# Performance work log

Measured on AMD Instinct MI355X. Metric: run time of the kernel, lower is better.

Reference implementation:

```python
import jax, jax.numpy as jnp
import numpy as np
import math

D_MODEL = 2048
D_STATE = 16
EXPAND = 2
D_INNER = D_MODEL * EXPAND          # 4096
DT_RANK = math.ceil(D_MODEL / 16)   # 128
BATCH, SEQ_LEN = 2, 512


def setup_inputs() -> dict:
    key = jax.random.key(0)
    ks = jax.random.split(key, 6)
    x = jax.random.normal(ks[0], (BATCH, SEQ_LEN, D_INNER), dtype=jnp.float32)
    # A_log such that A = -exp(A_log) is a stable negative-real decay
    A_log = jnp.log(jax.random.uniform(ks[1], (D_INNER, D_STATE), minval=0.5, maxval=16.0, dtype=jnp.float32))
    D = jnp.ones((D_INNER,), dtype=jnp.float32)
    x_proj_w = 0.02 * jax.random.normal(ks[2], (DT_RANK + 2 * D_STATE, D_INNER), dtype=jnp.float32)
    dt_init_std = DT_RANK ** -0.5
    dt_proj_w = jax.random.uniform(ks[3], (D_INNER, DT_RANK), minval=-dt_init_std, maxval=dt_init_std, dtype=jnp.float32)
    # inverse-softplus init of dt bias, dt ~ loguniform[1e-3, 0.1]
    dt = jnp.exp(jax.random.uniform(ks[4], (D_INNER,), dtype=jnp.float32) * (math.log(0.1) - math.log(0.001)) + math.log(0.001))
    dt = jnp.clip(dt, 1e-4, None)
    dt_proj_b = dt + jnp.log(-jnp.expm1(-dt))
    return {"x": x, "A_log": A_log, "D": D, "x_proj_w": x_proj_w,
            "dt_proj_w": dt_proj_w, "dt_proj_b": dt_proj_b}


def reference(x, A_log, D, x_proj_w, dt_proj_w, dt_proj_b):
    # x: (b, l, d)
    A = -jnp.exp(A_log)                                  # (d, n)
    xp = jnp.einsum('bld,rd->blr', x, x_proj_w)          # (b, l, dt_rank + 2n)
    dt_in = xp[..., :DT_RANK]
    B = xp[..., DT_RANK:DT_RANK + D_STATE]               # (b, l, n)
    C = xp[..., DT_RANK + D_STATE:]                      # (b, l, n)
    dt = jax.nn.softplus(jnp.einsum('blr,dr->bld', dt_in, dt_proj_w) + dt_proj_b)  # (b, l, d)
    dA = jnp.exp(dt[..., None] * A)                      # (b, l, d, n)
    dBx = dt[..., None] * B[:, :, None, :] * x[..., None]  # (b, l, d, n)

    def step(h, inp):
        dA_t, dBx_t, C_t = inp                           # (b,d,n), (b,d,n), (b,n)
        h = dA_t * h + dBx_t
        y = jnp.einsum('bdn,bn->bd', h, C_t)
        return h, y

    h0 = jnp.zeros((x.shape[0], D_INNER, D_STATE), dtype=x.dtype)
    _, ys = jax.lax.scan(step, h0,
                         (jnp.moveaxis(dA, 1, 0), jnp.moveaxis(dBx, 1, 0), jnp.moveaxis(C, 1, 0)))
    y = jnp.moveaxis(ys, 0, 1) + D * x                   # (b, l, d)
    return y
```

## Files before the change

### kernel.cpp

```cpp
#include <hip/hip_runtime.h>
#include <math.h>

#define BATCH   2
#define SEQLEN  512
#define DI      4096
#define DS      16
#define RDT     128
#define RTOT    160
#define BL      1024

#define KSPLIT  32
#define KSL     (DI / KSPLIT)

typedef __bf16 bf16;
typedef bf16  bf16x8 __attribute__((ext_vector_type(8)));
typedef bf16  bf16x4 __attribute__((ext_vector_type(4)));
typedef float f32x4  __attribute__((ext_vector_type(4)));

__global__ __launch_bounds__(256) void cast_both(const float* __restrict__ W,
                                                 const float* __restrict__ dtw,
                                                 bf16* __restrict__ Wb,
                                                 bf16* __restrict__ dtwb) {
  const int i = blockIdx.x * 256 + threadIdx.x;
  const float4* src;
  bf16* dst;
  int j;
  if (i < RTOT * DI / 4) { src = (const float4*)W;   dst = Wb;   j = i; }
  else                   { src = (const float4*)dtw; dst = dtwb; j = i - RTOT * DI / 4; }
  float4 v = src[j];
  bf16x4 o;
  o[0] = (bf16)v.x; o[1] = (bf16)v.y; o[2] = (bf16)v.z; o[3] = (bf16)v.w;
  *(bf16x4*)(dst + 4 * (size_t)j) = o;
}

__global__ __launch_bounds__(256) void gemm_xp_mfma(const float* __restrict__ x,
                                                    const bf16* __restrict__ Wb,
                                                    float* __restrict__ part) {
  const int tid = threadIdx.x;
  const int w = tid >> 6;
  const int lane = tid & 63;
  const int m = lane & 15;
  const int q = lane >> 4;
  const int row0 = blockIdx.x * 64 + 16 * w;
  const int k0 = blockIdx.y * KSL;

  f32x4 acc[10] = {};

  const float* ap = x + (size_t)(row0 + m) * DI + k0 + 8 * q;
  const bf16*  bp = Wb + (size_t)m * DI + k0 + 8 * q;

#pragma unroll
  for (int kk = 0; kk < KSL; kk += 32) {
    float4 a0 = *(const float4*)(ap + kk);
    float4 a1 = *(const float4*)(ap + kk + 4);
    bf16x8 af;
    af[0] = (bf16)a0.x; af[1] = (bf16)a0.y; af[2] = (bf16)a0.z; af[3] = (bf16)a0.w;
    af[4] = (bf16)a1.x; af[5] = (bf16)a1.y; af[6] = (bf16)a1.z; af[7] = (bf16)a1.w;
#pragma unroll
    for (int nt = 0; nt < 10; ++nt) {
      bf16x8 bfv = *(const bf16x8*)(bp + (size_t)nt * 16 * DI + kk);
      acc[nt] = __builtin_amdgcn_mfma_f32_16x16x32_bf16(af, bfv, acc[nt], 0, 0, 0);
    }
  }

  float* p = part + (size_t)blockIdx.y * (BL * RTOT);
#pragma unroll
  for (int nt = 0; nt < 10; ++nt)
#pragma unroll
    for (int r = 0; r < 4; ++r)
      p[(size_t)(row0 + 4 * q + r) * RTOT + nt * 16 + m] = acc[nt][r];
}

__global__ __launch_bounds__(256) void reduce_xp(const float* __restrict__ part,
                                                 float* __restrict__ BCf,
                                                 bf16* __restrict__ dtinb) {
  const int o = (blockIdx.x * 256 + threadIdx.x) * 4;
  float4 s = make_float4(0.f, 0.f, 0.f, 0.f);
#pragma unroll
  for (int k = 0; k < KSPLIT; ++k) {
    float4 v = *(const float4*)&part[(size_t)k * (BL * RTOT) + o];
    s.x += v.x; s.y += v.y; s.z += v.z; s.w += v.w;
  }
  const int row = o / RTOT;
  const int col = o - row * RTOT;
  if (col < RDT) {
    bf16x4 ob;
    ob[0] = (bf16)s.x; ob[1] = (bf16)s.y; ob[2] = (bf16)s.z; ob[3] = (bf16)s.w;
    *(bf16x4*)(dtinb + (size_t)row * RDT + col) = ob;
  } else {
    *(float4*)&BCf[(size_t)row * 32 + (col - RDT)] = s;
  }
}

__device__ __forceinline__ float row16_reduce_add(float p) {
  p += __int_as_float(__builtin_amdgcn_update_dpp(
      0, __float_as_int(p), 0x111, 0xf, 0xf, true));
  p += __int_as_float(__builtin_amdgcn_update_dpp(
      0, __float_as_int(p), 0x112, 0xf, 0xf, true));
  p += __int_as_float(__builtin_amdgcn_update_dpp(
      0, __float_as_int(p), 0x114, 0xf, 0xf, true));
  p += __int_as_float(__builtin_amdgcn_update_dpp(
      0, __float_as_int(p), 0x118, 0xf, 0xf, true));
  return p;
}

#define TC  64
#define TCP 68
#define NCH (SEQLEN / TC)

__global__ __launch_bounds__(256) void scan_fused(const float* __restrict__ x,
                                                  const float* __restrict__ A_log,
                                                  const float* __restrict__ Dvec,
                                                  const float* __restrict__ BCf,
                                                  const bf16* __restrict__ dtin,
                                                  const bf16* __restrict__ dtwb,
                                                  const float* __restrict__ dtb,
                                                  float* __restrict__ out) {
  __shared__ __align__(16) float dtS[16][TCP];
  __shared__ __align__(16) float xS[16][TCP];
  __shared__ __align__(16) float BS[16][TCP];
  __shared__ __align__(16) float CS[16][TCP];
  __shared__ __align__(16) float yS[TC][16];

  const int bid = blockIdx.x;
  const int b = bid >> 8;
  const int d0 = (bid & 255) * 16;
  const int tid = threadIdx.x;
  const int n = tid & 15;
  const int dc = tid >> 4;
  const int d = d0 + dc;
  const int w = tid >> 6;
  const int m = tid & 15;
  const int q = (tid >> 4) & 3;

  const float A = -expf(A_log[d * DS + n]);
  const float Dd = Dvec[d];
  const float bias = dtb[d0 + m];

  bf16x8 bfragW[4];
#pragma unroll
  for (int k = 0; k < 4; ++k)
    bfragW[k] = *(const bf16x8*)(dtwb + (size_t)(d0 + m) * RDT + 32 * k + 8 * q);

  const int lt = tid >> 2;
  const int lf = (tid & 3) * 4;
  const int rowbase = b * SEQLEN;

  bf16x8 afrag[4];
  float4 rx, rB, rC;
  {
    const int arow = rowbase + 16 * w + m;
#pragma unroll
    for (int k = 0; k < 4; ++k)
      afrag[k] = *(const bf16x8*)(dtin + (size_t)arow * RDT + 32 * k + 8 * q);
    const int row = rowbase + lt;
    rx = *(const float4*)&x[(size_t)row * DI + d0 + lf];
    rB = *(const float4*)&BCf[row * 32 + lf];
    rC = *(const float4*)&BCf[row * 32 + 16 + lf];
  }

  float h = 0.f;

  for (int c = 0; c < NCH; ++c) {
    if (c > 0) __syncthreads();

    {
      f32x4 acc = {};
#pragma unroll
      for (int k = 0; k < 4; ++k)
        acc = __builtin_amdgcn_mfma_f32_16x16x32_bf16(afrag[k], bfragW[k], acc, 0, 0, 0);
#pragma unroll
      for (int r = 0; r < 4; ++r) {
        const float z = acc[r] + bias;
        dtS[m][16 * w + 4 * q + r] = (z > 20.f) ? z : __logf(1.f + __expf(z));
      }
    }
    {
      const float rxa[4] = {rx.x, rx.y, rx.z, rx.w};
      const float rBa[4] = {rB.x, rB.y, rB.z, rB.w};
      const float rCa[4] = {rC.x, rC.y, rC.z, rC.w};
#pragma unroll
      for (int j = 0; j < 4; ++j) {
        xS[lf + j][lt] = rxa[j];
        BS[lf + j][lt] = rBa[j];
        CS[lf + j][lt] = rCa[j];
      }
    }
    if (c > 0) {
      const int prow = rowbase + (c - 1) * TC + lt;
      float4 yv = *(const float4*)&yS[lt][lf];
      *(float4*)&out[(size_t)prow * DI + d0 + lf] = yv;
    }

    __syncthreads();

    if (c < NCH - 1) {
      const int arow = rowbase + (c + 1) * TC + 16 * w + m;
#pragma unroll
      for (int k = 0; k < 4; ++k)
        afrag[k] = *(const bf16x8*)(dtin + (size_t)arow * RDT + 32 * k + 8 * q);
      const int row = rowbase + (c + 1) * TC + lt;
      rx = *(const float4*)&x[(size_t)row * DI + d0 + lf];
      rB = *(const float4*)&BCf[row * 32 + lf];
      rC = *(const float4*)&BCf[row * 32 + 16 + lf];
    }

    for (int g = 0; g < 8; ++g) {
      const int t0 = 8 * g;
      const float4 dv0 = *(const float4*)&dtS[dc][t0];
      const float4 dv1 = *(const float4*)&dtS[dc][t0 + 4];
      const float4 xv0 = *(const float4*)&xS[dc][t0];
      const float4 xv1 = *(const float4*)&xS[dc][t0 + 4];
      const float4 Bv0 = *(const float4*)&BS[n][t0];
      const float4 Bv1 = *(const float4*)&BS[n][t0 + 4];
      const float4 Cv0 = *(const float4*)&CS[n][t0];
      const float4 Cv1 = *(const float4*)&CS[n][t0 + 4];
      const float dt[8] = {dv0.x, dv0.y, dv0.z, dv0.w, dv1.x, dv1.y, dv1.z, dv1.w};
      const float xv[8] = {xv0.x, xv0.y, xv0.z, xv0.w, xv1.x, xv1.y, xv1.z, xv1.w};
      const float Bv[8] = {Bv0.x, Bv0.y, Bv0.z, Bv0.w, Bv1.x, Bv1.y, Bv1.z, Bv1.w};
      const float Cv[8] = {Cv0.x, Cv0.y, Cv0.z, Cv0.w, Cv1.x, Cv1.y, Cv1.z, Cv1.w};

      float e[8], u[8], p[8];
#pragma unroll
      for (int j = 0; j < 8; ++j) {
        e[j] = __expf(dt[j] * A);
        u[j] = dt[j] * xv[j] * Bv[j];
      }
#pragma unroll
      for (int j = 0; j < 8; ++j) {
        h = fmaf(e[j], h, u[j]);
        p[j] = h * Cv[j];
      }
#pragma unroll
      for (int j = 0; j < 8; ++j)
        p[j] = row16_reduce_add(p[j]);
      if (n == 15) {
#pragma unroll
        for (int j = 0; j < 8; ++j)
          yS[t0 + j][dc] = fmaf(Dd, xv[j], p[j]);
      }
    }
  }

  __syncthreads();
  {
    const int prow = rowbase + (NCH - 1) * TC + lt;
    float4 yv = *(const float4*)&yS[lt][lf];
    *(float4*)&out[(size_t)prow * DI + d0 + lf] = yv;
  }
}

extern "C" void kernel_launch(void* const* d_in, const int* in_sizes, int n_in,
                              void* d_out, int out_size, void* d_ws, size_t ws_size,
                              hipStream_t stream) {
  const float* x     = (const float*)d_in[0];
  const float* A_log = (const float*)d_in[1];
  const float* Dv    = (const float*)d_in[2];
  const float* W     = (const float*)d_in[3];
  const float* dtw   = (const float*)d_in[4];
  const float* dtb   = (const float*)d_in[5];
  float* out = (float*)d_out;

  char* ws = (char*)d_ws;
  float* part  = (float*)ws;
  bf16*  Wb    = (bf16*)(ws + 20971520);
  bf16*  dtwb  = (bf16*)(ws + 22282240);
  float* BCf   = (float*)(ws + 23330816);
  bf16*  dtinb = (bf16*)(ws + 23461888);

  cast_both<<<dim3(1152), 256, 0, stream>>>(W, dtw, Wb, dtwb);
  gemm_xp_mfma<<<dim3(16, KSPLIT), 256, 0, stream>>>(x, Wb, part);
  reduce_xp<<<dim3(160), 256, 0, stream>>>(part, BCf, dtinb);
  scan_fused<<<dim3(512), 256, 0, stream>>>(x, A_log, Dv, BCf, dtinb, dtwb, dtb, out);
}
```

Before: 137.6 us.

## Replace split-K partials and reduce kernel with in-block reduction plus atomics

Drops the weight cast kernel and the separate split-K reduction. The GEMM now converts fp32 weights to bf16 in registers, reduces its four waves' partial sums through shared memory, and atomically adds the result into a zeroed fp32 xp buffer. This removes the 20MB partial-sum write and read. The scan reads fp32 xp directly, converts it to bf16 per chunk, and folds log2e into the weights and A so it can use exp2/log2, and it fully unrolls the inner group loop. The atomics make summation order nondeterministic, and the scan now reloads wider fp32 fragments.

Measured after the change: 147.3 us. 1.07x slower.

```diff
diff --git a/kernel.cpp b/kernel.cpp
--- a/kernel.cpp
+++ b/kernel.cpp
@@ -9,86 +9,81 @@
 #define RTOT    160
 #define BL      1024
 
-#define KSPLIT  32
-#define KSL     (DI / KSPLIT)
+#define LOG2E 1.44269504088896340736f
+#define LN2   0.69314718055994530942f
 
 typedef __bf16 bf16;
 typedef bf16  bf16x8 __attribute__((ext_vector_type(8)));
-typedef bf16  bf16x4 __attribute__((ext_vector_type(4)));
 typedef float f32x4  __attribute__((ext_vector_type(4)));
 
-__global__ __launch_bounds__(256) void cast_both(const float* __restrict__ W,
-                                                 const float* __restrict__ dtw,
-                                                 bf16* __restrict__ Wb,
-                                                 bf16* __restrict__ dtwb) {
+__device__ __forceinline__ bf16x8 cvt8(const float4 a, const float4 b) {
+  bf16x8 r;
+  r[0] = (bf16)a.x; r[1] = (bf16)a.y; r[2] = (bf16)a.z; r[3] = (bf16)a.w;
+  r[4] = (bf16)b.x; r[5] = (bf16)b.y; r[6] = (bf16)b.z; r[7] = (bf16)b.w;
+  return r;
+}
+
+__device__ __forceinline__ bf16x8 cvt8s(const float4 a, const float4 b, const float s) {
+  bf16x8 r;
+  r[0] = (bf16)(s * a.x); r[1] = (bf16)(s * a.y); r[2] = (bf16)(s * a.z); r[3] = (bf16)(s * a.w);
+  r[4] = (bf16)(s * b.x); r[5] = (bf16)(s * b.y); r[6] = (bf16)(s * b.z); r[7] = (bf16)(s * b.w);
+  return r;
+}
+
+__global__ __launch_bounds__(256) void zero_xp(float* __restrict__ xp) {
   const int i = blockIdx.x * 256 + threadIdx.x;
-  const float4* src;
-  bf16* dst;
-  int j;
-  if (i < RTOT * DI / 4) { src = (const float4*)W;   dst = Wb;   j = i; }
-  else                   { src = (const float4*)dtw; dst = dtwb; j = i - RTOT * DI / 4; }
-  float4 v = src[j];
-  bf16x4 o;
-  o[0] = (bf16)v.x; o[1] = (bf16)v.y; o[2] = (bf16)v.z; o[3] = (bf16)v.w;
-  *(bf16x4*)(dst + 4 * (size_t)j) = o;
-}
-
-__global__ __launch_bounds__(256) void gemm_xp_mfma(const float* __restrict__ x,
-                                                    const bf16* __restrict__ Wb,
-                                                    float* __restrict__ part) {
+  *(float4*)&xp[4 * (size_t)i] = make_float4(0.f, 0.f, 0.f, 0.f);
+}
+
+#define MT    16
+#define KS    8
+#define LPAD  168
+
+__global__ __launch_bounds__(256, 2) void gemm_xp(const float* __restrict__ x,
+                                                  const float* __restrict__ W,
+                                                  float* __restrict__ xp) {
+  __shared__ float Lred[4][MT * LPAD];
   const int tid = threadIdx.x;
   const int w = tid >> 6;
   const int lane = tid & 63;
   const int m = lane & 15;
   const int q = lane >> 4;
-  const int row0 = blockIdx.x * 64 + 16 * w;
-  const int k0 = blockIdx.y * KSL;
+  const int row0 = blockIdx.x * MT;
+  const int k0 = blockIdx.y * (DI / KS) + w * 128;
 
   f32x4 acc[10] = {};
-
   const float* ap = x + (size_t)(row0 + m) * DI + k0 + 8 * q;
-  const bf16*  bp = Wb + (size_t)m * DI + k0 + 8 * q;
-
-#pragma unroll
-  for (int kk = 0; kk < KSL; kk += 32) {
+  const float* wp = W + (size_t)m * DI + k0 + 8 * q;
+
+#pragma unroll
+  for (int kk = 0; kk < 128; kk += 32) {
     float4 a0 = *(const float4*)(ap + kk);
     float4 a1 = *(const float4*)(ap + kk + 4);
-    bf16x8 af;
-    af[0] = (bf16)a0.x; af[1] = (bf16)a0.y; af[2] = (bf16)a0.z; af[3] = (bf16)a0.w;
-    af[4] = (bf16)a1.x; af[5] = (bf16)a1.y; af[6] = (bf16)a1.z; af[7] = (bf16)a1.w;
+    bf16x8 af = cvt8(a0, a1);
 #pragma unroll
     for (int nt = 0; nt < 10; ++nt) {
-      bf16x8 bfv = *(const bf16x8*)(bp + (size_t)nt * 16 * DI + kk);
-      acc[nt] = __builtin_amdgcn_mfma_f32_16x16x32_bf16(af, bfv, acc[nt], 0, 0, 0);
-    }
-  }
-
-  float* p = part + (size_t)blockIdx.y * (BL * RTOT);
+      const float* wq = wp + (size_t)nt * 16 * DI + kk;
+      float4 b0 = *(const float4*)(wq);
+      float4 b1 = *(const float4*)(wq + 4);
+      acc[nt] = __builtin_amdgcn_mfma_f32_16x16x32_bf16(af, cvt8(b0, b1), acc[nt], 0, 0, 0);
+    }
+  }
+
 #pragma unroll
   for (int nt = 0; nt < 10; ++nt)
 #pragma unroll
     for (int r = 0; r < 4; ++r)
-      p[(size_t)(row0 + 4 * q + r) * RTOT + nt * 16 + m] = acc[nt][r];
-}
-
-__global__ __launch_bounds__(256) void reduce_xp(const float* __restrict__ part,
-                                                 float* __restrict__ BCf,
-                                                 bf16* __restrict__ dtinb) {
-  const int o = (blockIdx.x * 256 + threadIdx.x) * 4;
-  float4 s = make_float4(0.f, 0.f, 0.f, 0.f);
-#pragma unroll
-  for (int k = 0; k < KSPLIT; ++k) {
-    float4 v = *(const float4*)&part[(size_t)k * (BL * RTOT) + o];
-    s.x += v.x; s.y += v.y; s.z += v.z; s.w += v.w;
-  }
-  const int row = o / RTOT;
-  const int col = o - row * RTOT;
-  if (col < RDT) {
-    bf16x4 ob;
-    ob[0] = (bf16)s.x; ob[1] = (bf16)s.y; ob[2] = (bf16)s.z; ob[3] = (bf16)s.w;
-    *(bf16x4*)(dtinb + (size_t)row * RDT + col) = ob;
-  } else {
-    *(float4*)&BCf[(size_t)row * 32 + (col - RDT)] = s;
+      Lred[w][(4 * q + r) * LPAD + nt * 16 + m] = acc[nt][r];
+  __syncthreads();
+
+#pragma unroll
+  for (int i = 0; i < 10; ++i) {
+    const int o = i * 256 + tid;
+    const int row = o / 160;
+    const int col = o - row * 160;
+    const int a = row * LPAD + col;
+    const float s = Lred[0][a] + Lred[1][a] + Lred[2][a] + Lred[3][a];
+    unsafeAtomicAdd(&xp[(size_t)(row0 + row) * RTOT + col], s);
   }
 }
 
@@ -108,14 +103,13 @@
 #define TCP 68
 #define NCH (SEQLEN / TC)
 
-__global__ __launch_bounds__(256) void scan_fused(const float* __restrict__ x,
-                                                  const float* __restrict__ A_log,
-                                                  const float* __restrict__ Dvec,
-                                                  const float* __restrict__ BCf,
-                                                  const bf16* __restrict__ dtin,
-                                                  const bf16* __restrict__ dtwb,
-                                                  const float* __restrict__ dtb,
-                                                  float* __restrict__ out) {
+__global__ __launch_bounds__(256, 2) void scan_fused(const float* __restrict__ x,
+                                                     const float* __restrict__ A_log,
+                                                     const float* __restrict__ Dvec,
+                                                     const float* __restrict__ xp,
+                                                     const float* __restrict__ dtw,
+                                                     const float* __restrict__ dtb,
+                                                     float* __restrict__ out) {
   __shared__ __align__(16) float dtS[16][TCP];
   __shared__ __align__(16) float xS[16][TCP];
   __shared__ __align__(16) float BS[16][TCP];
@@ -133,30 +127,37 @@
   const int m = tid & 15;
   const int q = (tid >> 4) & 3;
 
-  const float A = -expf(A_log[d * DS + n]);
+  const float A2 = -LOG2E * __expf(A_log[d * DS + n]);
   const float Dd = Dvec[d];
-  const float bias = dtb[d0 + m];
+  const float bias2 = dtb[d0 + m] * LOG2E;
 
   bf16x8 bfragW[4];
 #pragma unroll
-  for (int k = 0; k < 4; ++k)
-    bfragW[k] = *(const bf16x8*)(dtwb + (size_t)(d0 + m) * RDT + 32 * k + 8 * q);
+  for (int k = 0; k < 4; ++k) {
+    const float* p = dtw + (size_t)(d0 + m) * RDT + 32 * k + 8 * q;
+    float4 w0 = *(const float4*)p;
+    float4 w1 = *(const float4*)(p + 4);
+    bfragW[k] = cvt8s(w0, w1, LOG2E);
+  }
 
   const int lt = tid >> 2;
   const int lf = (tid & 3) * 4;
   const int rowbase = b * SEQLEN;
 
-  bf16x8 afrag[4];
+  float4 a0[4], a1[4];
   float4 rx, rB, rC;
   {
     const int arow = rowbase + 16 * w + m;
 #pragma unroll
-    for (int k = 0; k < 4; ++k)
-      afrag[k] = *(const bf16x8*)(dtin + (size_t)arow * RDT + 32 * k + 8 * q);
+    for (int k = 0; k < 4; ++k) {
+      const float* p = xp + (size_t)arow * RTOT + 32 * k + 8 * q;
+      a0[k] = *(const float4*)p;
+      a1[k] = *(const float4*)(p + 4);
+    }
     const int row = rowbase + lt;
     rx = *(const float4*)&x[(size_t)row * DI + d0 + lf];
-    rB = *(const float4*)&BCf[row * 32 + lf];
-    rC = *(const float4*)&BCf[row * 32 + 16 + lf];
+    rB = *(const float4*)&xp[(size_t)row * RTOT + RDT + lf];
+    rC = *(const float4*)&xp[(size_t)row * RTOT + RDT + 16 + lf];
   }
 
   float h = 0.f;
@@ -168,11 +169,12 @@
       f32x4 acc = {};
 #pragma unroll
       for (int k = 0; k < 4; ++k)
-        acc = __builtin_amdgcn_mfma_f32_16x16x32_bf16(afrag[k], bfragW[k], acc, 0, 0, 0);
+        acc = __builtin_amdgcn_mfma_f32_16x16x32_bf16(cvt8(a0[k], a1[k]), bfragW[k], acc, 0, 0, 0);
 #pragma unroll
       for (int r = 0; r < 4; ++r) {
-        const float z = acc[r] + bias;
-        dtS[m][16 * w + 4 * q + r] = (z > 20.f) ? z : __logf(1.f + __expf(z));
+        const float z2 = acc[r] + bias2;
+        dtS[m][16 * w + 4 * q + r] = (z2 > 28.854f) ? z2 * LN2
+                                   : LN2 * __log2f(1.f + exp2f(z2));
       }
     }
     {
@@ -197,14 +199,18 @@
     if (c < NCH - 1) {
       const int arow = rowbase + (c + 1) * TC + 16 * w + m;
 #pragma unroll
-      for (int k = 0; k < 4; ++k)
-        afrag[k] = *(const bf16x8*)(dtin + (size_t)arow * RDT + 32 * k + 8 * q);
+      for (int k = 0; k < 4; ++k) {
+        const float* p = xp + (size_t)arow * RTOT + 32 * k + 8 * q;
+        a0[k] = *(const float4*)p;
+        a1[k] = *(const float4*)(p + 4);
+      }
       const int row = rowbase + (c + 1) * TC + lt;
       rx = *(const float4*)&x[(size_t)row * DI + d0 + lf];
-      rB = *(const float4*)&BCf[row * 32 + lf];
-      rC = *(const float4*)&BCf[row * 32 + 16 + lf];
-    }
-
+      rB = *(const float4*)&xp[(size_t)row * RTOT + RDT + lf];
+      rC = *(const float4*)&xp[(size_t)row * RTOT + RDT + 16 + lf];
+    }
+
+#pragma unroll
     for (int g = 0; g < 8; ++g) {
       const int t0 = 8 * g;
       const float4 dv0 = *(const float4*)&dtS[dc][t0];
@@ -223,7 +229,7 @@
       float e[8], u[8], p[8];
 #pragma unroll
       for (int j = 0; j < 8; ++j) {
-        e[j] = __expf(dt[j] * A);
+        e[j] = exp2f(dt[j] * A2);
         u[j] = dt[j] * xv[j] * Bv[j];
       }
 #pragma unroll
@@ -261,15 +267,9 @@
   const float* dtb   = (const float*)d_in[5];
   float* out = (float*)d_out;
 
-  char* ws = (char*)d_ws;
-  float* part  = (float*)ws;
-  bf16*  Wb    = (bf16*)(ws + 20971520);
-  bf16*  dtwb  = (bf16*)(ws + 22282240);
-  float* BCf   = (float*)(ws + 23330816);
-  bf16*  dtinb = (bf16*)(ws + 23461888);
-
-  cast_both<<<dim3(1152), 256, 0, stream>>>(W, dtw, Wb, dtwb);
-  gemm_xp_mfma<<<dim3(16, KSPLIT), 256, 0, stream>>>(x, Wb, part);
-  reduce_xp<<<dim3(160), 256, 0, stream>>>(part, BCf, dtinb);
-  scan_fused<<<dim3(512), 256, 0, stream>>>(x, A_log, Dv, BCf, dtinb, dtwb, dtb, out);
-}
+  float* xp = (float*)d_ws;
+
+  zero_xp<<<dim3(160), 256, 0, stream>>>(xp);
+  gemm_xp<<<dim3(64, KS), 256, 0, stream>>>(x, W, xp);
+  scan_fused<<<dim3(512), 256, 0, stream>>>(x, A_log, Dv, xp, dtw, dtb, out);
+}
```
